# Kernel tuning notes

Hardware: AMD Instinct MI355X
Metric: run time of the kernel (lower is better)

Reference implementation:

```python
import jax, jax.numpy as jnp
import numpy as np

D_MODEL = 1024
N_HEAD = 16
D_HEAD = D_MODEL // N_HEAD
B, S = 4, 2048


def setup_inputs() -> dict:
    key = jax.random.key(0)
    ks = jax.random.split(key, 10)
    def xavier(k, shape):
        fan_in, fan_out = shape[1], shape[0]
        limit = np.sqrt(6.0 / (fan_in + fan_out))
        return jax.random.uniform(k, shape, jnp.float32, -limit, limit)
    x = jax.random.normal(ks[0], (B, S, D_MODEL), jnp.float32)
    mask = jnp.tril(jnp.ones((S, S), jnp.int32))[None, None]  # causal [1,1,S,S]
    return {
        "x": x,
        "Wq": xavier(ks[1], (D_MODEL, D_MODEL)), "bq": jnp.zeros((D_MODEL,), jnp.float32),
        "Wk": xavier(ks[2], (D_MODEL, D_MODEL)), "bk": jnp.zeros((D_MODEL,), jnp.float32),
        "Wv": xavier(ks[3], (D_MODEL, D_MODEL)), "bv": jnp.zeros((D_MODEL,), jnp.float32),
        "Wo": xavier(ks[4], (D_MODEL, D_MODEL)), "bo": jnp.zeros((D_MODEL,), jnp.float32),
        "mask": mask,
    }


def reference(x, Wq, bq, Wk, bk, Wv, bv, Wo, bo, mask):
    b, s, d = x.shape
    # Linear layers use y = x @ W.T + b (torch convention)
    def proj(W, bias):
        y = jnp.einsum('bsd,ed->bse', x, W) + bias
        return y.reshape(b, s, N_HEAD, D_HEAD).transpose(0, 2, 1, 3)  # [B,H,S,Dh]
    q = proj(Wq, bq)
    k = proj(Wk, bk)
    v = proj(Wv, bv)
    scores = jnp.einsum('bhqd,bhkd->bhqk', q, k) / jnp.sqrt(jnp.float32(D_HEAD))
    scores = jnp.where(mask == 0, jnp.float32(-1e9), scores)
    attn = jax.nn.softmax(scores, axis=-1)  # dropout is identity at eval
    context = jnp.einsum('bhqk,bhkd->bhqd', attn, v)
    context = context.transpose(0, 2, 1, 3).reshape(b, s, d)
    return jnp.einsum('bsd,ed->bse', context, Wo) + bo
```

## Files before the change

kernel.cpp:

```cpp
#include <hip/hip_runtime.h>
#include <stdint.h>

#define D_MODEL 1024
#define NHEAD   16
#define DHEAD   64
#define BATCH   4
#define SEQ     2048
#define MTOT    (BATCH*SEQ)

typedef __attribute__((ext_vector_type(4))) float f32x4;
typedef __attribute__((ext_vector_type(8))) short bf16x8;

typedef __attribute__((address_space(3))) uint32_t lds_u32;
typedef const __attribute__((address_space(1))) uint32_t glb_u32;

__device__ static inline void gload_lds16(const void* g, void* l) {
    __builtin_amdgcn_global_load_lds((glb_u32*)g, (lds_u32*)l, 16, 0, 0);
}

__device__ static inline ushort f2bf(float f) {
    uint32_t u = __builtin_bit_cast(uint32_t, f);
    u += 0x7fffu + ((u >> 16) & 1u);
    return (ushort)(u >> 16);
}

__device__ static inline float exp2_fast(float x) {
    float r; asm("v_exp_f32 %0, %1" : "=v"(r) : "v"(x)); return r;
}
__device__ static inline uint32_t cvt_pk_bf16(float a, float b) {
    uint32_t r;
    asm("v_cvt_pk_bf16_f32 %0, %1, %2" : "=v"(r) : "v"(a), "v"(b));
    return r;
}

__global__ __launch_bounds__(256) void convert_kernel(
    const float4* __restrict__ x,
    const float4* __restrict__ wq, const float4* __restrict__ wk,
    const float4* __restrict__ wv, const float4* __restrict__ wo,
    ushort4* __restrict__ xb, ushort4* __restrict__ wb)
{
    const int NX4 = (MTOT * D_MODEL) / 4;
    const int NW4 = (D_MODEL * D_MODEL) / 4;
    const int TOT = NX4 + 4 * NW4;
    for (int i = blockIdx.x * blockDim.x + threadIdx.x; i < TOT;
         i += gridDim.x * blockDim.x) {
        float4 v; ushort4* dst;
        if (i < NX4) { v = x[i]; dst = &xb[i]; }
        else {
            int j = i - NX4;
            int w = j >> 18;
            int r = j & (NW4 - 1);
            const float4* s = (w == 0) ? wq : (w == 1) ? wk : (w == 2) ? wv : wo;
            v = s[r]; dst = &wb[(size_t)w * NW4 + r];
        }
        ushort4 o;
        o.x = f2bf(v.x); o.y = f2bf(v.y); o.z = f2bf(v.z); o.w = f2bf(v.w);
        *dst = o;
    }
}

__global__ __launch_bounds__(256) void gemm_qkv(
    const ushort* __restrict__ A,
    const ushort* __restrict__ W3,
    const float* __restrict__ bq, const float* __restrict__ bk,
    const float* __restrict__ bv,
    ushort* __restrict__ Qb, ushort* __restrict__ Kb, ushort* __restrict__ Vtb,
    float qscale)
{
    __shared__ __align__(16) ushort As[128 * 32];
    __shared__ __align__(16) ushort Bs[128 * 32];

    const int tid = threadIdx.x;
    const int w  = tid >> 6, l = tid & 63, lo = l & 15, hi = l >> 4;
    const int wr = w >> 1, wc = w & 1;

    const int id = blockIdx.x;
    const int mb = ((id & 7) << 3) | ((id >> 3) & 7);
    const int nb = id >> 6;
    const int m0 = mb * 128, n0 = nb * 128;

    f32x4 acc[4][4] = {};
    const int srow = l >> 2;
    const int sk   = (l & 3) * 8;

    for (int kt = 0; kt < 32; ++kt) {
        const int k0 = kt * 32;
        __syncthreads();
#pragma unroll
        for (int c = 0; c < 2; ++c) {
            const int row = c * 64 + w * 16 + srow;
            gload_lds16(&A[(size_t)(m0 + row) * 1024 + k0 + sk],
                        &As[(c * 64 + w * 16) * 32]);
            gload_lds16(&W3[(size_t)(n0 + row) * 1024 + k0 + sk],
                        &Bs[(c * 64 + w * 16) * 32]);
        }
        __syncthreads();

        bf16x8 af[4], bfr[4];
#pragma unroll
        for (int mi = 0; mi < 4; ++mi)
            af[mi] = *(const bf16x8*)&As[(wr * 64 + mi * 16 + lo) * 32 + hi * 8];
#pragma unroll
        for (int ni = 0; ni < 4; ++ni)
            bfr[ni] = *(const bf16x8*)&Bs[(wc * 64 + ni * 16 + lo) * 32 + hi * 8];
#pragma unroll
        for (int mi = 0; mi < 4; ++mi)
#pragma unroll
            for (int ni = 0; ni < 4; ++ni)
                acc[mi][ni] = __builtin_amdgcn_mfma_f32_16x16x32_bf16(
                    af[mi], bfr[ni], acc[mi][ni], 0, 0, 0);
    }

    const int region = nb >> 3;
    const float scale = (region == 0) ? qscale : 1.0f;
    const float* bias = (region == 0) ? bq : (region == 1) ? bk : bv;
    ushort* outQK = (region == 0) ? Qb : Kb;

#pragma unroll
    for (int mi = 0; mi < 4; ++mi) {
#pragma unroll
        for (int ni = 0; ni < 4; ++ni) {
            const int gj  = n0 + wc * 64 + ni * 16 + lo;
            const int lcl = gj & 1023;
            const int h = lcl >> 6, dh = lcl & 63;
            const float bj = bias[lcl];
            if (region < 2) {
#pragma unroll
                for (int r = 0; r < 4; ++r) {
                    const int gi = m0 + wr * 64 + mi * 16 + hi * 4 + r;
                    const int b = gi >> 11, s = gi & (SEQ - 1);
                    outQK[(((size_t)(b * NHEAD + h)) * SEQ + s) * DHEAD + dh] =
                        f2bf((acc[mi][ni][r] + bj) * scale);
                }
            } else {
                const int gi0 = m0 + wr * 64 + mi * 16 + hi * 4;
                const int b = gi0 >> 11, s = gi0 & (SEQ - 1);
                ushort4 o4;
                o4.x = f2bf(acc[mi][ni][0] + bj);
                o4.y = f2bf(acc[mi][ni][1] + bj);
                o4.z = f2bf(acc[mi][ni][2] + bj);
                o4.w = f2bf(acc[mi][ni][3] + bj);
                *(ushort4*)&Vtb[(((size_t)(b * NHEAD + h)) * DHEAD + dh) * SEQ + s] = o4;
            }
        }
    }
}

__global__ __launch_bounds__(256) void gemm_out(
    const ushort* __restrict__ A,
    const ushort* __restrict__ W,
    const float*  __restrict__ bias,
    float* __restrict__ out)
{
    __shared__ __align__(16) ushort As[128 * 32];
    __shared__ __align__(16) ushort Bs[128 * 32];

    const int tid = threadIdx.x;
    const int w  = tid >> 6, l = tid & 63, lo = l & 15, hi = l >> 4;
    const int wr = w >> 1, wc = w & 1;

    const int id = blockIdx.y * 8 + blockIdx.x;
    const int mb = ((id & 7) << 3) | ((id >> 3) & 7);
    const int nb = id >> 6;
    const int m0 = mb * 128, n0 = nb * 128;

    f32x4 acc[4][4] = {};
    const int srow = l >> 2;
    const int sk   = (l & 3) * 8;

    for (int kt = 0; kt < 32; ++kt) {
        const int k0 = kt * 32;
        __syncthreads();
#pragma unroll
        for (int c = 0; c < 2; ++c) {
            const int row = c * 64 + w * 16 + srow;
            gload_lds16(&A[(size_t)(m0 + row) * 1024 + k0 + sk],
                        &As[(c * 64 + w * 16) * 32]);
            gload_lds16(&W[(size_t)(n0 + row) * 1024 + k0 + sk],
                        &Bs[(c * 64 + w * 16) * 32]);
        }
        __syncthreads();

        bf16x8 af[4], bfr[4];
#pragma unroll
        for (int mi = 0; mi < 4; ++mi)
            af[mi] = *(const bf16x8*)&As[(wr * 64 + mi * 16 + lo) * 32 + hi * 8];
#pragma unroll
        for (int ni = 0; ni < 4; ++ni)
            bfr[ni] = *(const bf16x8*)&Bs[(wc * 64 + ni * 16 + lo) * 32 + hi * 8];
#pragma unroll
        for (int mi = 0; mi < 4; ++mi)
#pragma unroll
            for (int ni = 0; ni < 4; ++ni)
                acc[mi][ni] = __builtin_amdgcn_mfma_f32_16x16x32_bf16(
                    af[mi], bfr[ni], acc[mi][ni], 0, 0, 0);
    }

#pragma unroll
    for (int mi = 0; mi < 4; ++mi)
#pragma unroll
        for (int ni = 0; ni < 4; ++ni) {
            const int gj = n0 + wc * 64 + ni * 16 + lo;
            const float bj = bias[gj];
#pragma unroll
            for (int r = 0; r < 4; ++r) {
                const int gi = m0 + wr * 64 + mi * 16 + hi * 4 + r;
                out[(size_t)gi * D_MODEL + gj] = acc[mi][ni][r] + bj;
            }
        }
}

__global__ __launch_bounds__(256) void attn_kernel(
    const ushort* __restrict__ Q, const ushort* __restrict__ K,
    const ushort* __restrict__ Vt, ushort* __restrict__ ctx)
{
    __shared__ __align__(16) ushort Ks[64 * 64];
    __shared__ __align__(16) ushort Vs[64 * 64];
    __shared__ __align__(16) ushort Pq[4 * 32 * 64];

    const int tid = threadIdx.x;
    const int w = tid >> 6, l = tid & 63, lo = l & 15, hi = l >> 4;
    const int sw = lo & 7;

    const int fid = blockIdx.x;
    const int xcd = fid & 7;
    const int u = fid >> 3;
    const int g = xcd * 8 + (u & 7);
    const int b = g >> 4, h = g & 15;
    const int j = u >> 3;
    const size_t base = (size_t)(b * NHEAD + h) * SEQ * DHEAD;

    const int krow = tid >> 3;
    const int kcol = (tid & 7) * 8;
    char* PqW = (char*)&Pq[w * 2048];

    for (int pass = 0; pass < 2; ++pass) {
        const int qt = pass ? (15 - j) : j;
        const int q0 = qt << 7;
        const int qw0 = q0 + w * 32;

        bf16x8 qf[2][2];
#pragma unroll
        for (int mi = 0; mi < 2; ++mi)
#pragma unroll
            for (int ks = 0; ks < 2; ++ks)
                qf[mi][ks] = *(const bf16x8*)&Q[base +
                    (size_t)(qw0 + mi * 16 + lo) * DHEAD + ks * 32 + hi * 8];

        f32x4 o[2][4] = {};
        float mrow[2] = {-1e30f, -1e30f}, lrow[2] = {0.f, 0.f};

        const int ntiles = (q0 + 128) >> 6;

        bf16x8 kregA[2], vregA[2], kregB[2], vregB[2];
#pragma unroll
        for (int c = 0; c < 2; ++c) {
            kregA[c] = *(const bf16x8*)&K[base + (size_t)(c * 32 + krow) * DHEAD + kcol];
            vregA[c] = *(const bf16x8*)&Vt[base + (size_t)(c * 32 + krow) * SEQ + kcol];
            kregB[c] = *(const bf16x8*)&K[base + (size_t)(64 + c * 32 + krow) * DHEAD + kcol];
            vregB[c] = *(const bf16x8*)&Vt[base + (size_t)(c * 32 + krow) * SEQ + 64 + kcol];
        }

        auto tile_body = [&](int t, bf16x8 (&KR)[2], bf16x8 (&VR)[2]) {
            const int kv0 = t << 6;
            __syncthreads();
#pragma unroll
            for (int c = 0; c < 2; ++c) {
                const int row = c * 32 + krow;
                const int g16 = (tid & 7) ^ (row & 7);
                *(bf16x8*)((char*)Ks + row * 128 + (g16 << 4)) = KR[c];
                *(bf16x8*)((char*)Vs + row * 128 + (g16 << 4)) = VR[c];
            }
            __syncthreads();
            if (t + 2 < ntiles) {
                const int nv0 = kv0 + 128;
#pragma unroll
                for (int c = 0; c < 2; ++c) {
                    KR[c] = *(const bf16x8*)&K[base + (size_t)(nv0 + c * 32 + krow) * DHEAD + kcol];
                    VR[c] = *(const bf16x8*)&Vt[base + (size_t)(c * 32 + krow) * SEQ + nv0 + kcol];
                }
            }
            if (kv0 > qw0 + 31) return;

            f32x4 s[2][4] = {};
            __builtin_amdgcn_s_setprio(1);
#pragma unroll
            for (int ks = 0; ks < 2; ++ks) {
                bf16x8 kf[4];
#pragma unroll
                for (int nj = 0; nj < 4; ++nj)
                    kf[nj] = *(const bf16x8*)((char*)Ks + (nj * 16 + lo) * 128 +
                                              ((((ks << 2) + hi) ^ sw) << 4));
#pragma unroll
                for (int mi = 0; mi < 2; ++mi)
#pragma unroll
                    for (int nj = 0; nj < 4; ++nj)
                        s[mi][nj] = __builtin_amdgcn_mfma_f32_16x16x32_bf16(
                            kf[nj], qf[mi][ks], s[mi][nj], 0, 0, 0);
            }
            __builtin_amdgcn_s_setprio(0);

            if (kv0 + 63 > qw0) {
#pragma unroll
                for (int mi = 0; mi < 2; ++mi) {
                    const int gq = qw0 + mi * 16 + lo;
#pragma unroll
                    for (int nj = 0; nj < 4; ++nj)
#pragma unroll
                        for (int r = 0; r < 4; ++r) {
                            const int gk = kv0 + nj * 16 + hi * 4 + r;
                            if (gk > gq) s[mi][nj][r] = -1e30f;
                        }
                }
            }

            float tl[2], corr[2];
#pragma unroll
            for (int mi = 0; mi < 2; ++mi) {
                float m = s[mi][0][0];
#pragma unroll
                for (int nj = 0; nj < 4; ++nj)
#pragma unroll
                    for (int r = 0; r < 4; ++r) m = fmaxf(m, s[mi][nj][r]);
                tl[mi] = m;
            }
            const bool grow = (tl[0] > mrow[0] + 8.f) | (tl[1] > mrow[1] + 8.f);
            if (__any(grow)) {
#pragma unroll
                for (int mi = 0; mi < 2; ++mi) {
                    float m2 = fmaxf(tl[mi], __shfl_xor(tl[mi], 16));
                    m2 = fmaxf(m2, __shfl_xor(m2, 32));
                    const float mn = fmaxf(mrow[mi], m2);
                    corr[mi] = exp2_fast(mrow[mi] - mn);
                    mrow[mi] = mn;
                }
#pragma unroll
                for (int mi = 0; mi < 2; ++mi)
#pragma unroll
                    for (int r = 0; r < 4; ++r) {
                        const float cb = __shfl(corr[mi], hi * 4 + r);
#pragma unroll
                        for (int ni = 0; ni < 4; ++ni) o[mi][ni][r] *= cb;
                    }
            } else { corr[0] = 1.f; corr[1] = 1.f; }

#pragma unroll
            for (int mi = 0; mi < 2; ++mi) {
                float ls = 0.f;
#pragma unroll
                for (int nj = 0; nj < 4; ++nj) {
#pragma unroll
                    for (int r = 0; r < 4; ++r) {
                        const float p = exp2_fast(s[mi][nj][r] - mrow[mi]);
                        s[mi][nj][r] = p;
                        ls += p;
                    }
                    uint2 pp;
                    pp.x = cvt_pk_bf16(s[mi][nj][0], s[mi][nj][1]);
                    pp.y = cvt_pk_bf16(s[mi][nj][2], s[mi][nj][3]);
                    const int gP = ((nj << 1) + (hi >> 1)) ^ sw;
                    *(uint2*)(PqW + (mi * 16 + lo) * 128 + (gP << 4) + ((hi & 1) << 3)) = pp;
                }
                ls += __shfl_xor(ls, 16);
                ls += __shfl_xor(ls, 32);
                lrow[mi] = lrow[mi] * corr[mi] + ls;
            }

            __builtin_amdgcn_s_setprio(1);
#pragma unroll
            for (int ks2 = 0; ks2 < 2; ++ks2) {
                bf16x8 pf[2], vf[4];
#pragma unroll
                for (int mi = 0; mi < 2; ++mi)
                    pf[mi] = *(const bf16x8*)(PqW + (mi * 16 + lo) * 128 +
                                              ((((ks2 << 2) + hi) ^ sw) << 4));
#pragma unroll
                for (int ni = 0; ni < 4; ++ni)
                    vf[ni] = *(const bf16x8*)((char*)Vs + (ni * 16 + lo) * 128 +
                                              ((((ks2 << 2) + hi) ^ sw) << 4));
#pragma unroll
                for (int mi = 0; mi < 2; ++mi)
#pragma unroll
                    for (int ni = 0; ni < 4; ++ni)
                        o[mi][ni] = __builtin_amdgcn_mfma_f32_16x16x32_bf16(
                            pf[mi], vf[ni], o[mi][ni], 0, 0, 0);
            }
            __builtin_amdgcn_s_setprio(0);
        };

        for (int tt = 0; tt < ntiles; tt += 2) {
            tile_body(tt,     kregA, vregA);
            tile_body(tt + 1, kregB, vregB);
        }

#pragma unroll
        for (int mi = 0; mi < 2; ++mi) {
            const float rv = 1.0f / lrow[mi];
#pragma unroll
            for (int r = 0; r < 4; ++r) {
                const float rb = __shfl(rv, hi * 4 + r);
                const int gq = qw0 + mi * 16 + hi * 4 + r;
#pragma unroll
                for (int ni = 0; ni < 4; ++ni)
                    ctx[((size_t)(b * SEQ + gq)) * D_MODEL + h * DHEAD + ni * 16 + lo] =
                        f2bf(o[mi][ni][r] * rb);
            }
        }
    }
}

extern "C" void kernel_launch(void* const* d_in, const int* in_sizes, int n_in,
                              void* d_out, int out_size, void* d_ws, size_t ws_size,
                              hipStream_t stream) {
    const float* x  = (const float*)d_in[0];
    const float* Wq = (const float*)d_in[1];
    const float* bq = (const float*)d_in[2];
    const float* Wk = (const float*)d_in[3];
    const float* bk = (const float*)d_in[4];
    const float* Wv = (const float*)d_in[5];
    const float* bv = (const float*)d_in[6];
    const float* Wo = (const float*)d_in[7];
    const float* bo = (const float*)d_in[8];

    char* ws = (char*)d_ws;
    ushort* xb  = (ushort*)(ws);
    ushort* wb  = (ushort*)(ws + (16u << 20));
    ushort* Qb  = (ushort*)(ws + (24u << 20));
    ushort* Kb  = (ushort*)(ws + (40u << 20));
    ushort* Vtb = (ushort*)(ws + (56u << 20));
    ushort* ctx = (ushort*)(ws + (72u << 20));

    convert_kernel<<<2048, 256, 0, stream>>>(
        (const float4*)x, (const float4*)Wq, (const float4*)Wk,
        (const float4*)Wv, (const float4*)Wo, (ushort4*)xb, (ushort4*)wb);

    const int NW = D_MODEL * D_MODEL;
    const float qscale = 0.125f * 1.44269504f;

    gemm_qkv<<<1536, 256, 0, stream>>>(xb, wb, bq, bk, bv, Qb, Kb, Vtb, qscale);

    attn_kernel<<<512, 256, 0, stream>>>(Qb, Kb, Vtb, ctx);

    gemm_out<<<dim3(8, 64), 256, 0, stream>>>(ctx, wb + 3 * NW, bo, (float*)d_out);
}
```

Baseline: 179.3 us.

## Pipeline GEMM K-loop with 4-stage LDS ring buffer and swizzled layout

Replaces the synchronous load-then-compute K-loop in both projection GEMMs with a 4-stage LDS ring buffer that prefetches three tiles ahead, using explicit vmcnt waits and a single barrier per iteration. It also XOR-swizzles the 16-byte chunks in LDS to reduce bank conflicts on fragment reads, and raises wave priority around the MFMA block. This is meant to hide global load latency and cut barrier stalls, at the cost of 64KB of LDS per block, which may lower occupancy. The output GEMM launch is flattened to a 1D grid.

```diff
diff --git a/kernel.cpp b/kernel.cpp
--- a/kernel.cpp
+++ b/kernel.cpp
@@ -59,6 +59,71 @@
     }
 }
 
+
+#define GSWZ(r) ((((r) >> 2) ^ (r)) & 3)
+
+#define GEMM_PIPE_BODY(APTR, BPTR)                                          \
+    __shared__ __align__(16) ushort S[4 * 2 * 4096]; \
+    const int tid = threadIdx.x;                                            \
+    const int w = tid >> 6, l = tid & 63, lo = l & 15, hi = l >> 4;         \
+    const int wr = w >> 1, wc = w & 1;                                      \
+    const int srow = l >> 2, gg = l & 3;                                    \
+    const int r0 = w * 16 + srow, r1 = 64 + w * 16 + srow;                  \
+    const int q0 = gg ^ GSWZ(r0), q1 = gg ^ GSWZ(r1);                       \
+    const ushort* aS0 = (APTR) + (size_t)(m0 + r0) * 1024 + q0 * 8;         \
+    const ushort* aS1 = (APTR) + (size_t)(m0 + r1) * 1024 + q1 * 8;         \
+    const ushort* bS0 = (BPTR) + (size_t)(n0 + r0) * 1024 + q0 * 8;         \
+    const ushort* bS1 = (BPTR) + (size_t)(n0 + r1) * 1024 + q1 * 8;         \
+    const int ldsA0 = (w * 16) * 32, ldsA1 = (64 + w * 16) * 32;            \
+    int offA[4], offB[4];                                                   \
+    _Pragma("unroll")                                                       \
+    for (int mi = 0; mi < 4; ++mi) {                                        \
+        const int rA = wr * 64 + mi * 16 + lo;                              \
+        offA[mi] = rA * 64 + ((hi ^ GSWZ(rA)) << 4);                        \
+        const int rB = wc * 64 + mi * 16 + lo;                              \
+        offB[mi] = rB * 64 + ((hi ^ GSWZ(rB)) << 4);                        \
+    }                                                                       \
+    f32x4 acc[4][4] = {};                                                   \
+    auto stage = [&](int st, int t) {                                       \
+        ushort* b = &S[st * 8192];                                          \
+        const int ko = t * 32;                                              \
+        gload_lds16(aS0 + ko, b + ldsA0);                                   \
+        gload_lds16(aS1 + ko, b + ldsA1);                                   \
+        gload_lds16(bS0 + ko, b + 4096 + ldsA0);                            \
+        gload_lds16(bS1 + ko, b + 4096 + ldsA1);                            \
+    };                                                                      \
+    stage(0, 0); stage(1, 1); stage(2, 2);                                  \
+    asm volatile("s_waitcnt vmcnt(8)" ::: "memory");                        \
+    __builtin_amdgcn_s_barrier();                                           \
+    __builtin_amdgcn_sched_barrier(0);                                      \
+    int st = 0;                                                             \
+    for (int t = 0; t < 32; ++t) {                                          \
+        if (t + 3 < 32) stage((st + 3) & 3, t + 3);                         \
+        const char* base = (const char*)&S[st * 8192];                      \
+        bf16x8 af[4], bfr[4];                                               \
+        _Pragma("unroll")                                                   \
+        for (int mi = 0; mi < 4; ++mi) {                                    \
+            af[mi]  = *(const bf16x8*)(base + offA[mi]);                    \
+            bfr[mi] = *(const bf16x8*)(base + 8192 + offB[mi]);             \
+        }                                                                   \
+        asm volatile("s_waitcnt lgkmcnt(0)" ::: "memory");                  \
+        __builtin_amdgcn_sched_barrier(0);                                  \
+        __builtin_amdgcn_s_setprio(1);                                      \
+        _Pragma("unroll")                                                   \
+        for (int mi = 0; mi < 4; ++mi)                                      \
+            _Pragma("unroll")                                               \
+            for (int ni = 0; ni < 4; ++ni)                                  \
+                acc[mi][ni] = __builtin_amdgcn_mfma_f32_16x16x32_bf16(      \
+                    af[mi], bfr[ni], acc[mi][ni], 0, 0, 0);                 \
+        __builtin_amdgcn_s_setprio(0);                                      \
+        if (t + 3 < 32)      { asm volatile("s_waitcnt vmcnt(8)" ::: "memory"); } \
+        else if (t == 29)    { asm volatile("s_waitcnt vmcnt(4)" ::: "memory"); } \
+        else if (t == 30)    { asm volatile("s_waitcnt vmcnt(0)" ::: "memory"); } \
+        __builtin_amdgcn_s_barrier();                                       \
+        __builtin_amdgcn_sched_barrier(0);                                  \
+        st = (st + 1) & 3;                                                  \
+    }
+
 __global__ __launch_bounds__(256) void gemm_qkv(
     const ushort* __restrict__ A,
     const ushort* __restrict__ W3,
@@ -67,49 +132,12 @@
     ushort* __restrict__ Qb, ushort* __restrict__ Kb, ushort* __restrict__ Vtb,
     float qscale)
 {
-    __shared__ __align__(16) ushort As[128 * 32];
-    __shared__ __align__(16) ushort Bs[128 * 32];
-
-    const int tid = threadIdx.x;
-    const int w  = tid >> 6, l = tid & 63, lo = l & 15, hi = l >> 4;
-    const int wr = w >> 1, wc = w & 1;
-
     const int id = blockIdx.x;
     const int mb = ((id & 7) << 3) | ((id >> 3) & 7);
     const int nb = id >> 6;
     const int m0 = mb * 128, n0 = nb * 128;
 
-    f32x4 acc[4][4] = {};
-    const int srow = l >> 2;
-    const int sk   = (l & 3) * 8;
-
-    for (int kt = 0; kt < 32; ++kt) {
-        const int k0 = kt * 32;
-        __syncthreads();
-#pragma unroll
-        for (int c = 0; c < 2; ++c) {
-            const int row = c * 64 + w * 16 + srow;
-            gload_lds16(&A[(size_t)(m0 + row) * 1024 + k0 + sk],
-                        &As[(c * 64 + w * 16) * 32]);
-            gload_lds16(&W3[(size_t)(n0 + row) * 1024 + k0 + sk],
-                        &Bs[(c * 64 + w * 16) * 32]);
-        }
-        __syncthreads();
-
-        bf16x8 af[4], bfr[4];
-#pragma unroll
-        for (int mi = 0; mi < 4; ++mi)
-            af[mi] = *(const bf16x8*)&As[(wr * 64 + mi * 16 + lo) * 32 + hi * 8];
-#pragma unroll
-        for (int ni = 0; ni < 4; ++ni)
-            bfr[ni] = *(const bf16x8*)&Bs[(wc * 64 + ni * 16 + lo) * 32 + hi * 8];
-#pragma unroll
-        for (int mi = 0; mi < 4; ++mi)
-#pragma unroll
-            for (int ni = 0; ni < 4; ++ni)
-                acc[mi][ni] = __builtin_amdgcn_mfma_f32_16x16x32_bf16(
-                    af[mi], bfr[ni], acc[mi][ni], 0, 0, 0);
-    }
+    GEMM_PIPE_BODY(A, W3)
 
     const int region = nb >> 3;
     const float scale = (region == 0) ? qscale : 1.0f;
@@ -152,49 +180,12 @@
     const float*  __restrict__ bias,
     float* __restrict__ out)
 {
-    __shared__ __align__(16) ushort As[128 * 32];
-    __shared__ __align__(16) ushort Bs[128 * 32];
-
-    const int tid = threadIdx.x;
-    const int w  = tid >> 6, l = tid & 63, lo = l & 15, hi = l >> 4;
-    const int wr = w >> 1, wc = w & 1;
-
-    const int id = blockIdx.y * 8 + blockIdx.x;
+    const int id = blockIdx.x;
     const int mb = ((id & 7) << 3) | ((id >> 3) & 7);
     const int nb = id >> 6;
     const int m0 = mb * 128, n0 = nb * 128;
 
-    f32x4 acc[4][4] = {};
-    const int srow = l >> 2;
-    const int sk   = (l & 3) * 8;
-
-    for (int kt = 0; kt < 32; ++kt) {
-        const int k0 = kt * 32;
-        __syncthreads();
-#pragma unroll
-        for (int c = 0; c < 2; ++c) {
-            const int row = c * 64 + w * 16 + srow;
-            gload_lds16(&A[(size_t)(m0 + row) * 1024 + k0 + sk],
-                        &As[(c * 64 + w * 16) * 32]);
-            gload_lds16(&W[(size_t)(n0 + row) * 1024 + k0 + sk],
-                        &Bs[(c * 64 + w * 16) * 32]);
-        }
-        __syncthreads();
-
-        bf16x8 af[4], bfr[4];
-#pragma unroll
-        for (int mi = 0; mi < 4; ++mi)
-            af[mi] = *(const bf16x8*)&As[(wr * 64 + mi * 16 + lo) * 32 + hi * 8];
-#pragma unroll
-        for (int ni = 0; ni < 4; ++ni)
-            bfr[ni] = *(const bf16x8*)&Bs[(wc * 64 + ni * 16 + lo) * 32 + hi * 8];
-#pragma unroll
-        for (int mi = 0; mi < 4; ++mi)
-#pragma unroll
-            for (int ni = 0; ni < 4; ++ni)
-                acc[mi][ni] = __builtin_amdgcn_mfma_f32_16x16x32_bf16(
-                    af[mi], bfr[ni], acc[mi][ni], 0, 0, 0);
-    }
+    GEMM_PIPE_BODY(A, W)
 
 #pragma unroll
     for (int mi = 0; mi < 4; ++mi)
@@ -441,5 +432,5 @@
 
     attn_kernel<<<512, 256, 0, stream>>>(Qb, Kb, Vtb, ctx);
 
-    gemm_out<<<dim3(8, 64), 256, 0, stream>>>(ctx, wb + 3 * NW, bo, (float*)d_out);
-}
+    gemm_out<<<512, 256, 0, stream>>>(ctx, wb + 3 * NW, bo, (float*)d_out);
+}
```

Result: faster. 171.4 us (-4.4%).
